# Kernel optimization log

Measured on AMD Instinct MI355X. Metric: run time of the kernel, lower is better.

Reference implementation:

```python
import jax, jax.numpy as jnp
import numpy as np

HIDDEN_SIZE = 256
INPUT_SIZE = 4
N_CLASSES = 2
START_VALUE_PADDING = -100.0


def setup_inputs() -> dict:
    key = jax.random.key(0)
    ks = jax.random.split(key, 11)
    B, T = 128, 2048
    H, IN = HIDDEN_SIZE, INPUT_SIZE
    s = 1.0 / np.sqrt(H)  # torch LSTM/Linear default init scale
    u = lambda k, shape: jax.random.uniform(k, shape, jnp.float32, -s, s)
    return {
        "y": jax.random.normal(ks[0], (B, T), dtype=jnp.float32),
        "W_ih0": u(ks[1], (4 * H, IN)),
        "W_hh0": u(ks[2], (4 * H, H)),
        "b_ih0": u(ks[3], (4 * H,)),
        "b_hh0": u(ks[4], (4 * H,)),
        "W_ih1": u(ks[5], (4 * H, H)),
        "W_hh1": u(ks[6], (4 * H, H)),
        "b_ih1": u(ks[7], (4 * H,)),
        "b_hh1": u(ks[8], (4 * H,)),
        "W_fc": u(ks[9], (N_CLASSES, H)),
        "b_fc": u(ks[10], (N_CLASSES,)),
    }


def _cell(x, h, c, W_ih, W_hh, b):
    # torch LSTM gate order: i, f, g, o
    g = x @ W_ih.T + h @ W_hh.T + b
    i, f, gg, o = jnp.split(g, 4, axis=-1)
    c = jax.nn.sigmoid(f) * c + jax.nn.sigmoid(i) * jnp.tanh(gg)
    h = jax.nn.sigmoid(o) * jnp.tanh(c)
    return h, c


def reference(y, W_ih0, W_hh0, b_ih0, b_hh0, W_ih1, W_hh1, b_ih1, b_hh1, W_fc, b_fc):
    B, T = y.shape
    H, IN = HIDDEN_SIZE, INPUT_SIZE
    # torch roll-on-padded-array windowing == prepend IN-1 pad values,
    # window t = [y_pre[t], ..., y_pre[t+IN-1]] (oldest-first, current sample last)
    y_pre = jnp.concatenate(
        [jnp.full((B, IN - 1), START_VALUE_PADDING, y.dtype), y], axis=1)
    idx = jnp.arange(T)[:, None] + jnp.arange(IN)[None, :]  # [T, IN]
    seq = y_pre[:, idx]  # [B, T, IN]

    b0 = b_ih0 + b_hh0
    b1 = b_ih1 + b_hh1

    def step(carry, x_t):
        h1, c1, h2, c2 = carry
        h1, c1 = _cell(x_t, h1, c1, W_ih0, W_hh0, b0)
        h2, c2 = _cell(h1, h2, c2, W_ih1, W_hh1, b1)
        return (h1, c1, h2, c2), h2

    z = jnp.zeros((B, H), y.dtype)
    _, hs = jax.lax.scan(step, (z, z, z, z), seq.transpose(1, 0, 2))  # hs: [T,B,H]
    lstm_out = hs.transpose(1, 0, 2)  # [B, T, H]
    out = lstm_out @ W_fc.T + b_fc  # [B, T, N_CLASSES]  (phase='train')
    return out
```

## Files before the change

### kernel.cpp

```cpp
#include <hip/hip_runtime.h>
#include <math.h>

#define T_LEN 2048
#define NGRP  32
#define NSLC  16
#define BPG   4
#define NTH   512

typedef __attribute__((ext_vector_type(8))) short short8v;
typedef __attribute__((ext_vector_type(4))) float f32x4;
typedef unsigned int u32t;
typedef unsigned long long u64t;

#define H1_OFF  0
#define H2_OFF  131072
#define ABT_OFF 262144
#define WS_U64  262145


__device__ __forceinline__ float fsigm(float x) {
  return __builtin_amdgcn_rcpf(1.0f + __builtin_amdgcn_exp2f(-1.44269504f * x));
}
__device__ __forceinline__ float ftanh(float x) {
  return fmaf(-2.0f, __builtin_amdgcn_rcpf(1.0f + __builtin_amdgcn_exp2f(2.88539009f * x)), 1.0f);
}

__device__ __forceinline__ u32t bf_rn(float x) {
  u32t b; __builtin_memcpy(&b, &x, 4);
  return (b + 0x7FFFu + ((b >> 16) & 1u)) >> 16;
}
__device__ __forceinline__ void split_bf(float x, u32t& hi, u32t& lo) {
  hi = bf_rn(x);
  u32t hb = hi << 16; float hf; __builtin_memcpy(&hf, &hb, 4);
  lo = bf_rn(x - hf);
}

__global__ void init_ws_kernel(u64t* ws) {
  for (int i = blockIdx.x * blockDim.x + threadIdx.x; i < WS_U64;
       i += gridDim.x * blockDim.x)
    ws[i] = 0ull;
}

#define MFMA16(a, b, c) __builtin_amdgcn_mfma_f32_16x16x32_bf16(a, b, c, 0, 0, 0)
#define ALD(ptr) __hip_atomic_load(ptr, __ATOMIC_RELAXED, __HIP_MEMORY_SCOPE_AGENT)

__launch_bounds__(NTH, 2)
__global__ void lstm_persist(const float* __restrict__ y,
                             const float* __restrict__ Wih0, const float* __restrict__ Whh0,
                             const float* __restrict__ bih0, const float* __restrict__ bhh0,
                             const float* __restrict__ Wih1, const float* __restrict__ Whh1,
                             const float* __restrict__ bih1, const float* __restrict__ bhh1,
                             const float* __restrict__ Wfc, const float* __restrict__ bfc,
                             float* __restrict__ out, u64t* wsu) {
  extern __shared__ char lds[];
  const int tid   = threadIdx.x;
  const int lane  = tid & 63;
  const int wid   = tid >> 6;
  const int slice = blockIdx.x & 15;
  const int gA    = blockIdx.x >> 4;
  const int gB    = gA + 16;

  u64t* h1b    = wsu + H1_OFF;
  u64t* h2b    = wsu + H2_OFF;
  u64t* abortf = wsu + ABT_OFF;

  for (int i = tid; i < 16384; i += NTH) ((u64t*)lds)[i] = 0ull;

  const bool isL1 = (wid >= 4);
  const int  m = lane & 15, kq4 = lane >> 4;
  const int  gate = m & 3, hs4 = m >> 2;
  const int  hidb = slice * 16 + (wid & 3) * 4;
  const int  grow = gate * 256 + hidb + hs4;

  const float* WA = isL1 ? Wih1 : Whh0;
  const float* WB = isL1 ? Whh1 : Wfc;
  const int   rowB   = isL1 ? grow : m;
  const bool  bValid = isL1 || (wid == 0 && m < 2);

  short8v ahi[16], alo[16];
  #pragma unroll
  for (int ks = 0; ks < 8; ++ks) {
    short8v h0, l0, h1, l1;
    #pragma unroll
    for (int j = 0; j < 8; ++j) {
      int k = ks * 32 + kq4 * 8 + j;
      u32t hi, lo;
      split_bf(WA[grow * 256 + k], hi, lo);
      h0[j] = (short)hi; l0[j] = (short)lo;
      float vb = bValid ? WB[rowB * 256 + k] : 0.f;
      split_bf(vb, hi, lo);
      h1[j] = (short)hi; l1[j] = (short)lo;
    }
    ahi[ks] = h0;     alo[ks] = l0;
    ahi[8 + ks] = h1; alo[8 + ks] = l1;
  }

  const int hidC = hidb + kq4;
  float bias4[4], wx[16];
  #pragma unroll
  for (int r = 0; r < 4; ++r) {
    int row = r * 256 + hidC;
    bias4[r] = isL1 ? (bih1[row] + bhh1[row]) : (bih0[row] + bhh0[row]);
    #pragma unroll
    for (int kk = 0; kk < 4; ++kk)
      wx[r * 4 + kk] = isL1 ? 0.f : Wih0[row * 4 + kk];
  }
  float bfc0 = 0.f, bfc1 = 0.f;
  if (wid == 0) { bfc0 = bfc[0]; bfc1 = bfc[1]; }
  const float* ybA = y + (gA * BPG + (m & 3)) * T_LEN;
  const float* ybB = y + (gB * BPG + (m & 3)) * T_LEN;

  float cstA = 0.f, cstB = 0.f;

  const int srow = tid >> 7;
  const int sc2  = (tid & 127) * 2;
  const int soff = srow * 512 + (((tid & 127) * 4) ^ (srow << 4));
  const int brow = lane & 15;
  const int bxr  = (brow & 7) << 4;
  const int bco  = kq4 * 16;

  u64t vA1[2], vA2[2], vB1[2], vB2[2];

  auto issue = [&](int G, int p, u64t* v1, u64t* v2) {
    if (p >= 1 && p <= T_LEN) {
      const u64t* s1 = h1b + (u64t)((p - 1) & 3) * (NGRP * 1024) + G * 1024 + srow * 256 + sc2;
      v1[0] = ALD(s1); v1[1] = ALD(s1 + 1);
    }
    if (p >= 2) {
      const u64t* s2 = h2b + (u64t)((p - 2) & 3) * (NGRP * 1024) + G * 1024 + srow * 256 + sc2;
      v2[0] = ALD(s2); v2[1] = ALD(s2 + 1);
    }
  };

  auto check_unpack = [&](char* LB, int G, int p, u64t* v1, u64t* v2) {
    const bool need1 = (p >= 1 && p <= T_LEN);
    const bool need2 = (p >= 2);
    const u64t* s1 = h1b + (u64t)((p - 1) & 3) * (NGRP * 1024) + G * 1024 + srow * 256 + sc2;
    const u64t* s2 = h2b + (u64t)((p - 2) & 3) * (NGRP * 1024) + G * 1024 + srow * 256 + sc2;
    const u32t tg1 = (u32t)(p + 15), tg2 = (u32t)(p + 14);
    u32t st = 0;
    if (need1) {
      if ((u32t)(v1[0] >> 32) != tg1) st |= 1u;
      if ((u32t)(v1[1] >> 32) != tg1) st |= 2u;
    }
    if (need2) {
      if ((u32t)(v2[0] >> 32) != tg2) st |= 4u;
      if ((u32t)(v2[1] >> 32) != tg2) st |= 8u;
    }
    int guard = 0;
    while (st) {
      __builtin_amdgcn_s_sleep(1);
      if (st & 1u) v1[0] = ALD(s1);
      if (st & 2u) v1[1] = ALD(s1 + 1);
      if (st & 4u) v2[0] = ALD(s2);
      if (st & 8u) v2[1] = ALD(s2 + 1);
      u32t n = 0;
      if ((st & 1u) && (u32t)(v1[0] >> 32) != tg1) n |= 1u;
      if ((st & 2u) && (u32t)(v1[1] >> 32) != tg1) n |= 2u;
      if ((st & 4u) && (u32t)(v2[0] >> 32) != tg2) n |= 4u;
      if ((st & 8u) && (u32t)(v2[1] >> 32) != tg2) n |= 8u;
      st = n;
      if (st) {
        if (++guard > (1 << 15)) {
          __hip_atomic_store(abortf, 1ull, __ATOMIC_RELAXED, __HIP_MEMORY_SCOPE_AGENT);
          break;
        }
        if ((guard & 31) == 0 &&
            __hip_atomic_load(abortf, __ATOMIC_RELAXED, __HIP_MEMORY_SCOPE_AGENT) != 0)
          break;
      }
    }
    char* sbase = LB + (p & 1) * 32768;
    if (need1) {
      u32t e0 = (u32t)v1[0], e1 = (u32t)v1[1];
      *(u32t*)(sbase + soff)        = (e0 >> 16) | (e1 & 0xFFFF0000u);
      *(u32t*)(sbase + 8192 + soff) = (e0 & 0xFFFFu) | (e1 << 16);
    }
    if (need2) {
      u32t e0 = (u32t)v2[0], e1 = (u32t)v2[1];
      *(u32t*)(sbase + 16384 + soff) = (e0 >> 16) | (e1 & 0xFFFF0000u);
      *(u32t*)(sbase + 24576 + soff) = (e0 & 0xFFFFu) | (e1 << 16);
    }
  };

#define BRD(sb, pl, ks) \
  (*(const short8v*)((sb) + (pl) * 8192 + brow * 512 + ((((ks) * 64) + bco) ^ bxr)))

  auto compute_fin = [&](char* LB, int G, int p, float& cst, const float* yb) {
    const bool need1 = (p >= 1 && p <= T_LEN);
    const bool act = isL1 ? need1 : (p < T_LEN);
    const char* sb = LB + (p & 1) * 32768;
    f32x4 accP = {0.f, 0.f, 0.f, 0.f}, accQ = {0.f, 0.f, 0.f, 0.f};
    if (act) {
      if (!isL1) {
        #pragma unroll
        for (int ks = 0; ks < 8; ++ks) {
          short8v bh = BRD(sb, 0, ks), bl = BRD(sb, 1, ks);
          accP = MFMA16(ahi[ks], bh, accP);
          accQ = MFMA16(ahi[ks], bl, accQ);
          accQ = MFMA16(alo[ks], bh, accQ);
        }
      } else {
        #pragma unroll
        for (int ks = 0; ks < 8; ++ks) {
          short8v b1h = BRD(sb, 0, ks), b1l = BRD(sb, 1, ks);
          short8v b2h = BRD(sb, 2, ks), b2l = BRD(sb, 3, ks);
          accP = MFMA16(ahi[ks], b1h, accP);
          accQ = MFMA16(ahi[ks], b1l, accQ);
          accQ = MFMA16(alo[ks], b1h, accQ);
          accP = MFMA16(ahi[8 + ks], b2h, accP);
          accQ = MFMA16(ahi[8 + ks], b2l, accQ);
          accQ = MFMA16(alo[8 + ks], b2h, accQ);
        }
      }
      float g[4];
      #pragma unroll
      for (int r = 0; r < 4; ++r) g[r] = accP[r] + accQ[r] + bias4[r];
      if (!isL1) {
        float xx[4];
        #pragma unroll
        for (int kk = 0; kk < 4; ++kk) {
          int ti = p + kk - 3;
          xx[kk] = (ti >= 0) ? yb[ti] : -100.0f;
        }
        #pragma unroll
        for (int kk = 0; kk < 4; ++kk)
          #pragma unroll
          for (int r = 0; r < 4; ++r) g[r] = fmaf(wx[r * 4 + kk], xx[kk], g[r]);
      }
      cst = fsigm(g[1]) * cst + fsigm(g[0]) * ftanh(g[2]);
      float hv = fsigm(g[3]) * ftanh(cst);
      if (m < BPG) {
        u32t hi, lo; split_bf(hv, hi, lo);
        const u32t tag = (u32t)(isL1 ? (p + 15) : (p + 16));
        u64t w = ((u64t)tag << 32) | (u64t)((hi << 16) | lo);
        u64t* dst = isL1
            ? (h2b + (u64t)((p - 1) & 3) * (NGRP * 1024) + G * 1024 + m * 256 + hidC)
            : (h1b + (u64t)(p & 3) * (NGRP * 1024) + G * 1024 + m * 256 + hidC);
        __hip_atomic_store(dst, w, __ATOMIC_RELAXED, __HIP_MEMORY_SCOPE_AGENT);
      }
    }
    if (wid == 0 && p >= 2 && slice == ((p - 2) & 15)) {
      f32x4 aF = {0.f, 0.f, 0.f, 0.f}, aG = {0.f, 0.f, 0.f, 0.f};
      #pragma unroll
      for (int ks = 0; ks < 8; ++ks) {
        short8v b2h = BRD(sb, 2, ks), b2l = BRD(sb, 3, ks);
        aF = MFMA16(ahi[8 + ks], b2h, aF);
        aG = MFMA16(ahi[8 + ks], b2l, aG);
        aG = MFMA16(alo[8 + ks], b2h, aG);
      }
      if (lane < BPG) {
        float2 o;
        o.x = aF[0] + aG[0] + bfc0;
        o.y = aF[1] + aG[1] + bfc1;
        *(float2*)(&out[(G * BPG + lane) * (T_LEN * 2) + (p - 2) * 2]) = o;
      }
    }
  };

  __syncthreads();

  for (int p = 0; p <= T_LEN + 1; ++p) {
    check_unpack(lds, gA, p, vA1, vA2);
    __syncthreads();
    issue(gB, p, vB1, vB2);
    compute_fin(lds, gA, p, cstA, ybA);
    check_unpack(lds + 65536, gB, p, vB1, vB2);
    __syncthreads();
    if (p <= T_LEN) issue(gA, p + 1, vA1, vA2);
    compute_fin(lds + 65536, gB, p, cstB, ybB);
  }
}

extern "C" void kernel_launch(void* const* d_in, const int* in_sizes, int n_in,
                              void* d_out, int out_size, void* d_ws, size_t ws_size,
                              hipStream_t stream) {
  const float* y    = (const float*)d_in[0];
  const float* Wih0 = (const float*)d_in[1];
  const float* Whh0 = (const float*)d_in[2];
  const float* bih0 = (const float*)d_in[3];
  const float* bhh0 = (const float*)d_in[4];
  const float* Wih1 = (const float*)d_in[5];
  const float* Whh1 = (const float*)d_in[6];
  const float* bih1 = (const float*)d_in[7];
  const float* bhh1 = (const float*)d_in[8];
  const float* Wfc  = (const float*)d_in[9];
  const float* bfc  = (const float*)d_in[10];
  float* out = (float*)d_out;
  u64t*  ws  = (u64t*)d_ws;

  (void)hipFuncSetAttribute(reinterpret_cast<const void*>(lstm_persist),
                            hipFuncAttributeMaxDynamicSharedMemorySize, 131072);

  hipLaunchKernelGGL(init_ws_kernel, dim3(256), dim3(256), 0, stream, ws);
  hipLaunchKernelGGL(lstm_persist, dim3(NGRP / 2 * NSLC), dim3(NTH), 131072, stream,
                     y, Wih0, Whh0, bih0, bhh0, Wih1, Whh1, bih1, bhh1,
                     Wfc, bfc, out, ws);
}
```

Before: 7.834 ms.

## Replace per-element tagged hidden-state polling with per-slice flags and 32-bit payloads

Inter-block synchronization moves from 64-bit words that carry a step tag, each polled individually, to 32-bit hidden-state words plus one progress flag per slice. A whole wave polls the flags with a single vote. The wait and the load of the other group's state are moved to sit between that group's MFMA work and its activation tail, and are unpacked into a ping-pong LDS buffer shared by the two groups. The aim is to halve global state traffic, cheapen polling, and overlap communication with compute. It relies on relaxed data stores becoming visible before the flag store, which adds a memory-ordering risk.

```diff
diff --git a/kernel.cpp b/kernel.cpp
--- a/kernel.cpp
+++ b/kernel.cpp
@@ -2,9 +2,6 @@
 #include <math.h>
 
 #define T_LEN 2048
-#define NGRP  32
-#define NSLC  16
-#define BPG   4
 #define NTH   512
 
 typedef __attribute__((ext_vector_type(8))) short short8v;
@@ -12,10 +9,14 @@
 typedef unsigned int u32t;
 typedef unsigned long long u64t;
 
-#define H1_OFF  0
-#define H2_OFF  131072
-#define ABT_OFF 262144
-#define WS_U64  262145
+#define HA1 0
+#define HA2 65536
+#define HB1 131072
+#define HB2 196608
+#define FLA 262144
+#define FLB 262656
+#define ABT 263168
+#define WS_U32 263169
 
 
 __device__ __forceinline__ float fsigm(float x) {
@@ -24,7 +25,6 @@
 __device__ __forceinline__ float ftanh(float x) {
   return fmaf(-2.0f, __builtin_amdgcn_rcpf(1.0f + __builtin_amdgcn_exp2f(2.88539009f * x)), 1.0f);
 }
-
 __device__ __forceinline__ u32t bf_rn(float x) {
   u32t b; __builtin_memcpy(&b, &x, 4);
   return (b + 0x7FFFu + ((b >> 16) & 1u)) >> 16;
@@ -35,14 +35,16 @@
   lo = bf_rn(x - hf);
 }
 
-__global__ void init_ws_kernel(u64t* ws) {
-  for (int i = blockIdx.x * blockDim.x + threadIdx.x; i < WS_U64;
+__global__ void init_ws_kernel(u32t* ws) {
+  for (int i = blockIdx.x * blockDim.x + threadIdx.x; i < WS_U32;
        i += gridDim.x * blockDim.x)
-    ws[i] = 0ull;
+    ws[i] = 0u;
 }
 
 #define MFMA16(a, b, c) __builtin_amdgcn_mfma_f32_16x16x32_bf16(a, b, c, 0, 0, 0)
-#define ALD(ptr) __hip_atomic_load(ptr, __ATOMIC_RELAXED, __HIP_MEMORY_SCOPE_AGENT)
+#define ALD32(ptr) __hip_atomic_load((ptr), __ATOMIC_RELAXED, __HIP_MEMORY_SCOPE_AGENT)
+#define ALD64(ptr) __hip_atomic_load((ptr), __ATOMIC_RELAXED, __HIP_MEMORY_SCOPE_AGENT)
+#define AST32(ptr, v) __hip_atomic_store((ptr), (v), __ATOMIC_RELAXED, __HIP_MEMORY_SCOPE_AGENT)
 
 __launch_bounds__(NTH, 2)
 __global__ void lstm_persist(const float* __restrict__ y,
@@ -51,20 +53,23 @@
                              const float* __restrict__ Wih1, const float* __restrict__ Whh1,
                              const float* __restrict__ bih1, const float* __restrict__ bhh1,
                              const float* __restrict__ Wfc, const float* __restrict__ bfc,
-                             float* __restrict__ out, u64t* wsu) {
+                             float* __restrict__ out, u32t* wsu) {
   extern __shared__ char lds[];
   const int tid   = threadIdx.x;
   const int lane  = tid & 63;
   const int wid   = tid >> 6;
+  const int gang  = blockIdx.x >> 4;
   const int slice = blockIdx.x & 15;
-  const int gA    = blockIdx.x >> 4;
-  const int gB    = gA + 16;
-
-  u64t* h1b    = wsu + H1_OFF;
-  u64t* h2b    = wsu + H2_OFF;
-  u64t* abortf = wsu + ABT_OFF;
-
-  for (int i = tid; i < 16384; i += NTH) ((u64t*)lds)[i] = 0ull;
+  const int gA    = gang;
+  const int gB    = gang + 16;
+
+  u32t* hA1 = wsu + HA1; u32t* hA2 = wsu + HA2;
+  u32t* hB1 = wsu + HB1; u32t* hB2 = wsu + HB2;
+  u32t* flgA = wsu + FLA + gang * 32;
+  u32t* flgB = wsu + FLB + gang * 32;
+  u32t* abortf = wsu + ABT;
+
+  for (int i = tid; i < 16384; i += NTH) ((u32t*)lds)[i] = 0u;
 
   const bool isL1 = (wid >= 4);
   const int  m = lane & 15, kq4 = lane >> 4;
@@ -107,8 +112,8 @@
   }
   float bfc0 = 0.f, bfc1 = 0.f;
   if (wid == 0) { bfc0 = bfc[0]; bfc1 = bfc[1]; }
-  const float* ybA = y + (gA * BPG + (m & 3)) * T_LEN;
-  const float* ybB = y + (gB * BPG + (m & 3)) * T_LEN;
+  const float* ybA = y + (gA * 4 + (m & 3)) * T_LEN;
+  const float* ybB = y + (gB * 4 + (m & 3)) * T_LEN;
 
   float cstA = 0.f, cstB = 0.f;
 
@@ -119,83 +124,22 @@
   const int bxr  = (brow & 7) << 4;
   const int bco  = kq4 * 16;
 
-  u64t vA1[2], vA2[2], vB1[2], vB2[2];
-
-  auto issue = [&](int G, int p, u64t* v1, u64t* v2) {
-    if (p >= 1 && p <= T_LEN) {
-      const u64t* s1 = h1b + (u64t)((p - 1) & 3) * (NGRP * 1024) + G * 1024 + srow * 256 + sc2;
-      v1[0] = ALD(s1); v1[1] = ALD(s1 + 1);
-    }
-    if (p >= 2) {
-      const u64t* s2 = h2b + (u64t)((p - 2) & 3) * (NGRP * 1024) + G * 1024 + srow * 256 + sc2;
-      v2[0] = ALD(s2); v2[1] = ALD(s2 + 1);
-    }
-  };
-
-  auto check_unpack = [&](char* LB, int G, int p, u64t* v1, u64t* v2) {
-    const bool need1 = (p >= 1 && p <= T_LEN);
-    const bool need2 = (p >= 2);
-    const u64t* s1 = h1b + (u64t)((p - 1) & 3) * (NGRP * 1024) + G * 1024 + srow * 256 + sc2;
-    const u64t* s2 = h2b + (u64t)((p - 2) & 3) * (NGRP * 1024) + G * 1024 + srow * 256 + sc2;
-    const u32t tg1 = (u32t)(p + 15), tg2 = (u32t)(p + 14);
-    u32t st = 0;
-    if (need1) {
-      if ((u32t)(v1[0] >> 32) != tg1) st |= 1u;
-      if ((u32t)(v1[1] >> 32) != tg1) st |= 2u;
-    }
-    if (need2) {
-      if ((u32t)(v2[0] >> 32) != tg2) st |= 4u;
-      if ((u32t)(v2[1] >> 32) != tg2) st |= 8u;
-    }
-    int guard = 0;
-    while (st) {
-      __builtin_amdgcn_s_sleep(1);
-      if (st & 1u) v1[0] = ALD(s1);
-      if (st & 2u) v1[1] = ALD(s1 + 1);
-      if (st & 4u) v2[0] = ALD(s2);
-      if (st & 8u) v2[1] = ALD(s2 + 1);
-      u32t n = 0;
-      if ((st & 1u) && (u32t)(v1[0] >> 32) != tg1) n |= 1u;
-      if ((st & 2u) && (u32t)(v1[1] >> 32) != tg1) n |= 2u;
-      if ((st & 4u) && (u32t)(v2[0] >> 32) != tg2) n |= 4u;
-      if ((st & 8u) && (u32t)(v2[1] >> 32) != tg2) n |= 8u;
-      st = n;
-      if (st) {
-        if (++guard > (1 << 15)) {
-          __hip_atomic_store(abortf, 1ull, __ATOMIC_RELAXED, __HIP_MEMORY_SCOPE_AGENT);
-          break;
-        }
-        if ((guard & 31) == 0 &&
-            __hip_atomic_load(abortf, __ATOMIC_RELAXED, __HIP_MEMORY_SCOPE_AGENT) != 0)
-          break;
-      }
-    }
-    char* sbase = LB + (p & 1) * 32768;
-    if (need1) {
-      u32t e0 = (u32t)v1[0], e1 = (u32t)v1[1];
-      *(u32t*)(sbase + soff)        = (e0 >> 16) | (e1 & 0xFFFF0000u);
-      *(u32t*)(sbase + 8192 + soff) = (e0 & 0xFFFFu) | (e1 << 16);
-    }
-    if (need2) {
-      u32t e0 = (u32t)v2[0], e1 = (u32t)v2[1];
-      *(u32t*)(sbase + 16384 + soff) = (e0 >> 16) | (e1 & 0xFFFF0000u);
-      *(u32t*)(sbase + 24576 + soff) = (e0 & 0xFFFFu) | (e1 << 16);
-    }
-  };
-
 #define BRD(sb, pl, ks) \
   (*(const short8v*)((sb) + (pl) * 8192 + brow * 512 + ((((ks) * 64) + bco) ^ bxr)))
 
-  auto compute_fin = [&](char* LB, int G, int p, float& cst, const float* yb) {
-    const bool need1 = (p >= 1 && p <= T_LEN);
-    const bool act = isL1 ? need1 : (p < T_LEN);
-    const char* sb = LB + (p & 1) * 32768;
+  auto section = [&](const char* sbR, char* sbW,
+                     u32t* sH1, u32t* sH2,
+                     const u32t* oH1, const u32t* oH2,
+                     u32t* pf, int sp, int qq,
+                     float& cst, const float* yb, int G) {
+    const bool act = isL1 ? (sp >= 1 && sp <= T_LEN) : (sp < T_LEN);
+
     f32x4 accP = {0.f, 0.f, 0.f, 0.f}, accQ = {0.f, 0.f, 0.f, 0.f};
     if (act) {
       if (!isL1) {
         #pragma unroll
         for (int ks = 0; ks < 8; ++ks) {
-          short8v bh = BRD(sb, 0, ks), bl = BRD(sb, 1, ks);
+          short8v bh = BRD(sbR, 0, ks), bl = BRD(sbR, 1, ks);
           accP = MFMA16(ahi[ks], bh, accP);
           accQ = MFMA16(ahi[ks], bl, accQ);
           accQ = MFMA16(alo[ks], bh, accQ);
@@ -203,8 +147,8 @@
       } else {
         #pragma unroll
         for (int ks = 0; ks < 8; ++ks) {
-          short8v b1h = BRD(sb, 0, ks), b1l = BRD(sb, 1, ks);
-          short8v b2h = BRD(sb, 2, ks), b2l = BRD(sb, 3, ks);
+          short8v b1h = BRD(sbR, 0, ks), b1l = BRD(sbR, 1, ks);
+          short8v b2h = BRD(sbR, 2, ks), b2l = BRD(sbR, 3, ks);
           accP = MFMA16(ahi[ks], b1h, accP);
           accQ = MFMA16(ahi[ks], b1l, accQ);
           accQ = MFMA16(alo[ks], b1h, accQ);
@@ -213,6 +157,31 @@
           accQ = MFMA16(alo[8 + ks], b2h, accQ);
         }
       }
+    }
+
+    const bool ld1 = (qq >= 1 && qq <= T_LEN);
+    const bool ld2 = (qq >= 2 && qq <= T_LEN + 1);
+    u64t v1 = 0, v2 = 0;
+    if (ld1 | ld2) {
+      const u32t tgt = (u32t)qq;
+      int guard = 0;
+      for (;;) {
+        u32t f = ALD32(&pf[lane & 15]);
+        if (__all((int)(f >= tgt || (lane & 15) == slice))) break;
+        if (++guard > (1 << 18)) {
+          AST32(abortf, 1u);
+          break;
+        }
+        if ((guard & 31) == 0 && ALD32(abortf) != 0) break;
+        __builtin_amdgcn_s_sleep(2);
+      }
+      if (ld1)
+        v1 = ALD64((const u64t*)(oH1 + ((qq - 1) & 3) * 16384 + gang * 1024 + srow * 256 + sc2));
+      if (ld2)
+        v2 = ALD64((const u64t*)(oH2 + ((qq - 2) & 3) * 16384 + gang * 1024 + srow * 256 + sc2));
+    }
+
+    if (act) {
       float g[4];
       #pragma unroll
       for (int r = 0; r < 4; ++r) g[r] = accP[r] + accQ[r] + bias4[r];
@@ -220,7 +189,7 @@
         float xx[4];
         #pragma unroll
         for (int kk = 0; kk < 4; ++kk) {
-          int ti = p + kk - 3;
+          int ti = sp + kk - 3;
           xx[kk] = (ti >= 0) ? yb[ti] : -100.0f;
         }
         #pragma unroll
@@ -230,45 +199,57 @@
       }
       cst = fsigm(g[1]) * cst + fsigm(g[0]) * ftanh(g[2]);
       float hv = fsigm(g[3]) * ftanh(cst);
-      if (m < BPG) {
+      if (m < 4) {
         u32t hi, lo; split_bf(hv, hi, lo);
-        const u32t tag = (u32t)(isL1 ? (p + 15) : (p + 16));
-        u64t w = ((u64t)tag << 32) | (u64t)((hi << 16) | lo);
-        u64t* dst = isL1
-            ? (h2b + (u64t)((p - 1) & 3) * (NGRP * 1024) + G * 1024 + m * 256 + hidC)
-            : (h1b + (u64t)(p & 3) * (NGRP * 1024) + G * 1024 + m * 256 + hidC);
-        __hip_atomic_store(dst, w, __ATOMIC_RELAXED, __HIP_MEMORY_SCOPE_AGENT);
-      }
-    }
-    if (wid == 0 && p >= 2 && slice == ((p - 2) & 15)) {
+        u32t pk = (hi << 16) | lo;
+        u32t* dst = isL1
+            ? (sH2 + ((sp - 1) & 3) * 16384 + gang * 1024 + m * 256 + hidC)
+            : (sH1 + (sp & 3) * 16384 + gang * 1024 + m * 256 + hidC);
+        AST32(dst, pk);
+      }
+    }
+
+    if (wid == 0 && sp >= 2 && slice == ((sp - 2) & 15)) {
       f32x4 aF = {0.f, 0.f, 0.f, 0.f}, aG = {0.f, 0.f, 0.f, 0.f};
       #pragma unroll
       for (int ks = 0; ks < 8; ++ks) {
-        short8v b2h = BRD(sb, 2, ks), b2l = BRD(sb, 3, ks);
+        short8v b2h = BRD(sbR, 2, ks), b2l = BRD(sbR, 3, ks);
         aF = MFMA16(ahi[8 + ks], b2h, aF);
         aG = MFMA16(ahi[8 + ks], b2l, aG);
         aG = MFMA16(alo[8 + ks], b2h, aG);
       }
-      if (lane < BPG) {
+      if (lane < 4) {
         float2 o;
         o.x = aF[0] + aG[0] + bfc0;
         o.y = aF[1] + aG[1] + bfc1;
-        *(float2*)(&out[(G * BPG + lane) * (T_LEN * 2) + (p - 2) * 2]) = o;
-      }
-    }
+        *(float2*)(&out[(G * 4 + lane) * (T_LEN * 2) + (sp - 2) * 2]) = o;
+      }
+    }
+
+    asm volatile("s_waitcnt vmcnt(0)" ::: "memory");
+    if (ld1) {
+      u32t e0 = (u32t)v1, e1 = (u32t)(v1 >> 32);
+      *(u32t*)(sbW + soff)        = (e0 >> 16) | (e1 & 0xFFFF0000u);
+      *(u32t*)(sbW + 8192 + soff) = (e0 & 0xFFFFu) | (e1 << 16);
+    }
+    if (ld2) {
+      u32t e0 = (u32t)v2, e1 = (u32t)(v2 >> 32);
+      *(u32t*)(sbW + 16384 + soff) = (e0 >> 16) | (e1 & 0xFFFF0000u);
+      *(u32t*)(sbW + 24576 + soff) = (e0 & 0xFFFFu) | (e1 << 16);
+    }
+    __syncthreads();
   };
 
+  char* LA = lds;
+  char* LB = lds + 32768;
+
   __syncthreads();
 
   for (int p = 0; p <= T_LEN + 1; ++p) {
-    check_unpack(lds, gA, p, vA1, vA2);
-    __syncthreads();
-    issue(gB, p, vB1, vB2);
-    compute_fin(lds, gA, p, cstA, ybA);
-    check_unpack(lds + 65536, gB, p, vB1, vB2);
-    __syncthreads();
-    if (p <= T_LEN) issue(gA, p + 1, vA1, vA2);
-    compute_fin(lds + 65536, gB, p, cstB, ybB);
+    if (tid == 0 && p > 0) AST32(&flgB[slice], (u32t)p);
+    section(LA, LB, hA1, hA2, hB1, hB2, flgB, p, p, cstA, ybA, gA);
+    if (tid == 0) AST32(&flgA[slice], (u32t)(p + 1));
+    section(LB, LA, hB1, hB2, hA1, hA2, flgA, p, p + 1, cstB, ybB, gB);
   }
 }
 
@@ -287,13 +268,13 @@
   const float* Wfc  = (const float*)d_in[9];
   const float* bfc  = (const float*)d_in[10];
   float* out = (float*)d_out;
-  u64t*  ws  = (u64t*)d_ws;
+  u32t*  ws  = (u32t*)d_ws;
 
   (void)hipFuncSetAttribute(reinterpret_cast<const void*>(lstm_persist),
                             hipFuncAttributeMaxDynamicSharedMemorySize, 131072);
 
   hipLaunchKernelGGL(init_ws_kernel, dim3(256), dim3(256), 0, stream, ws);
-  hipLaunchKernelGGL(lstm_persist, dim3(NGRP / 2 * NSLC), dim3(NTH), 131072, stream,
+  hipLaunchKernelGGL(lstm_persist, dim3(256), dim3(NTH), 131072, stream,
                      y, Wih0, Whh0, bih0, bhh0, Wih1, Whh1, bih1, bhh1,
                      Wfc, bfc, out, ws);
 }
```

Result: slower. 9.877 ms (+26.1%).
